# Kernel optimization log

Hardware: AMD Instinct MI355X
Metric: run time of the kernel (lower is better)

## Reference

```python
import jax, jax.numpy as jnp
import numpy as np
from jax.ops import segment_sum

N = 100000   # nodes
E = 1600000  # edges
D = 128      # input feature dim
H = 128      # hidden dim
S = 64       # substructure ids
G = 512      # graphs in batch
EPS = 1e-5


def setup_inputs() -> dict:
    key = jax.random.key(0)
    ks = jax.random.split(key, 12)
    subst_ids = jax.random.randint(ks[0], (N,), 0, S)
    x = jax.random.normal(ks[1], (N, D), dtype=jnp.float32)
    # column 5 carries the integer substructure id, as in data.x[:, 5].long()
    x = x.at[:, 5].set(subst_ids.astype(jnp.float32))
    edge_index = jax.random.randint(ks[2], (2, E), 0, N)
    batch = jnp.sort(jax.random.randint(ks[3], (N,), 0, G))
    s = 0.05  # weight scale to keep activations sane
    return {
        "x": x,
        "edge_index": edge_index,
        "subst_ids": subst_ids,
        "batch": batch,
        "attn_w1": jax.random.normal(ks[4], (D, 64), jnp.float32) * s,
        "attn_b1": jnp.zeros((64,), jnp.float32),
        "attn_w2": jax.random.normal(ks[5], (64, 1), jnp.float32) * s,
        "conv_w0": jax.random.normal(ks[6], (D + 1, H), jnp.float32) * s,
        "conv_b0": jnp.zeros((H,), jnp.float32),
        "conv_w1": jax.random.normal(ks[7], (H, H), jnp.float32) * s,
        "conv_b1": jnp.zeros((H,), jnp.float32),
        "conv_w2": jax.random.normal(ks[8], (H, H), jnp.float32) * s,
        "conv_b2": jnp.zeros((H,), jnp.float32),
        "conv_w3": jax.random.normal(ks[9], (H, H), jnp.float32) * s,
        "conv_b3": jnp.zeros((H,), jnp.float32),
        "bn_gamma": jnp.ones((4, H), jnp.float32),
        "bn_beta": jnp.zeros((4, H), jnp.float32),
        "bn_rmean": jnp.zeros((4, H), jnp.float32),
        "bn_rvar": jnp.ones((4, H), jnp.float32),
        "head_w1": jax.random.normal(ks[10], (H, H // 2), jnp.float32) * s,
        "head_b1": jnp.zeros((H // 2,), jnp.float32),
        "head_w2": jax.random.normal(ks[11], (H // 2, 1), jnp.float32) * s,
        "head_b2": jnp.zeros((1,), jnp.float32),
    }


def _gcn_conv(x, src, dst, dinv, w, b):
    # PyG GCNConv with self-loops: out[dst] += d^-1/2_src d^-1/2_dst (xW)[src]
    h = x @ w                                   # [N, H]
    coef = dinv[src] * dinv[dst]                # [E]
    agg = segment_sum(h[src] * coef[:, None], dst, num_segments=N)
    agg = agg + h * (dinv * dinv)[:, None]      # self-loop term
    return agg + b


def reference(x, edge_index, subst_ids, batch,
              attn_w1, attn_b1, attn_w2,
              conv_w0, conv_b0, conv_w1, conv_b1, conv_w2, conv_b2, conv_w3, conv_b3,
              bn_gamma, bn_beta, bn_rmean, bn_rvar,
              head_w1, head_b1, head_w2, head_b2):
    # --- substructure attention ---
    ones_n = jnp.ones((N,), x.dtype)
    cnt = jnp.maximum(segment_sum(ones_n, subst_ids, num_segments=S), 1.0)
    subst_mean = segment_sum(x, subst_ids, num_segments=S) / cnt[:, None]  # [S, D]
    scores = jnp.tanh(subst_mean @ attn_w1 + attn_b1) @ attn_w2            # [S, 1]
    subst_attn = jax.nn.softmax(scores, axis=0)                            # [S, 1]
    atom_attn = subst_attn[subst_ids]                                      # [N, 1]
    h = jnp.concatenate([x, atom_attn], axis=1)                            # [N, D+1]

    # --- shared symmetric normalization (self-loops included) ---
    src, dst = edge_index[0], edge_index[1]
    deg = segment_sum(jnp.ones((E,), x.dtype), dst, num_segments=N) + 1.0
    dinv = jax.lax.rsqrt(deg)

    convs = [(conv_w0, conv_b0), (conv_w1, conv_b1), (conv_w2, conv_b2), (conv_w3, conv_b3)]
    for i, (w, b) in enumerate(convs):
        h = _gcn_conv(h, src, dst, dinv, w, b)
        # BatchNorm1d in eval mode
        h = (h - bn_rmean[i]) * jax.lax.rsqrt(bn_rvar[i] + EPS) * bn_gamma[i] + bn_beta[i]
        h = jax.nn.elu(h) if i < 3 else jax.nn.relu(h)
        # dropout p=0.3 is identity in inference

    # --- global mean pool over graphs ---
    gcnt = jnp.maximum(segment_sum(jnp.ones((N,), x.dtype), batch, num_segments=G), 1.0)
    pooled = segment_sum(h, batch, num_segments=G) / gcnt[:, None]         # [G, H]

    # --- prediction head (dropout off) ---
    z = jax.nn.elu(pooled @ head_w1 + head_b1)
    return z @ head_w2 + head_b2                                            # [G, 1]
```

## Files before the change

### kernel.cpp

```cpp
#include <hip/hip_runtime.h>
#include <cmath>

#define NN 100000
#define EE 1600000
#define DD 128
#define HH 128
#define SS 64
#define GG 512

#define NBE 782
#define EBK 196
#define EHS 800

typedef float f32x4 __attribute__((ext_vector_type(4)));
typedef short s16x8 __attribute__((ext_vector_type(8)));

constexpr size_t alignup(size_t x){ return (x + 255) & ~(size_t)255; }
constexpr size_t SZ_P16   = (size_t)NN*64*sizeof(unsigned);
constexpr size_t OFF_HW   = 0;
constexpr size_t OFF_H    = alignup(OFF_HW + SZ_P16);
constexpr size_t OFF_CSRS = alignup(OFF_H + SZ_P16);
constexpr size_t OFF_ROW  = alignup(OFF_CSRS + (size_t)EE*4);
constexpr size_t OFF_DINV = alignup(OFF_ROW + (size_t)(NN+1)*4);
constexpr size_t OFF_SATT = alignup(OFF_DINV + (size_t)NN*4);
constexpr size_t OFF_GST  = alignup(OFF_SATT + 64*4);
constexpr size_t OFF_BH   = alignup(OFF_GST + 513*4);
constexpr size_t OFF_BO   = alignup(OFF_BH + (size_t)64*400*4);
constexpr size_t OFF_TOT  = alignup(OFF_BO + (size_t)64*400*4);
constexpr size_t OFF_ROW2 = alignup(OFF_TOT + 64*4);
constexpr size_t OFF_LIST = alignup(OFF_ROW2 + 65*4);
constexpr size_t OFF_W16  = alignup(OFF_LIST + (size_t)NN*4);
constexpr size_t OFF_EH   = alignup(OFF_W16 + (size_t)3*8192*4);
constexpr size_t OFF_EB   = alignup(OFF_EH + (size_t)EBK*EHS*4);
constexpr size_t OFF_ET   = alignup(OFF_EB + (size_t)EBK*EHS*4);
constexpr size_t OFF_EBASE= alignup(OFF_ET + EBK*4);
constexpr size_t OFF_DSTE = alignup(OFF_EBASE + 200*4);
constexpr size_t OFF_SRCE = alignup(OFF_DSTE + (size_t)EE*4);
constexpr size_t OFF_POOL = alignup(OFF_SRCE + (size_t)EE*4);
constexpr size_t OFF_GSUM = alignup(OFF_POOL + (size_t)GG*HH*4);
constexpr size_t OFF_END  = alignup(OFF_GSUM + (size_t)SS*DD*4);
constexpr size_t ZERO_BEG   = OFF_POOL;
constexpr size_t ZERO_BYTES = OFF_END - OFF_POOL;

__device__ __forceinline__ unsigned pack2bf(float a, float b){
  unsigned ua = __float_as_uint(a); ua += 0x7fffu + ((ua >> 16) & 1u);
  unsigned ub = __float_as_uint(b); ub += 0x7fffu + ((ub >> 16) & 1u);
  return (ua >> 16) | (ub & 0xffff0000u);
}
__device__ __forceinline__ float bf_lo(unsigned u){ return __uint_as_float(u << 16); }
__device__ __forceinline__ float bf_hi(unsigned u){ return __uint_as_float(u & 0xffff0000u); }
__device__ __forceinline__ s16x8 as_s16x8(uint4 v){ union { uint4 u; s16x8 s; } x; x.u = v; return x.s; }

__global__ __launch_bounds__(256) void hist_kernel(const int* __restrict__ sid, int* __restrict__ bhist)
{
  __shared__ int h[64];
  int t = threadIdx.x, b = blockIdx.x;
  if (t < 64) h[t] = 0;
  __syncthreads();
  int n = b*256 + t;
  if (n < NN) atomicAdd(&h[sid[n]], 1);
  __syncthreads();
  if (t < 64) bhist[t*400 + b] = h[t];
}

__global__ __launch_bounds__(512) void offs_kernel(const int* __restrict__ bhist, int* __restrict__ boff2, int* __restrict__ tots)
{
  __shared__ int sh[512];
  int s = blockIdx.x, t = threadIdx.x;
  int v = (t < 391) ? bhist[s*400 + t] : 0;
  sh[t] = v;
  __syncthreads();
  for (int off = 1; off < 512; off <<= 1) {
    int u = (t >= off) ? sh[t - off] : 0;
    __syncthreads();
    sh[t] += u;
    __syncthreads();
  }
  if (t < 391) boff2[s*400 + t] = sh[t] - v;
  if (t == 511) tots[s] = sh[511];
}

__global__ __launch_bounds__(64) void base_kernel(const int* __restrict__ tots, int* __restrict__ row2)
{
  int l = threadIdx.x;
  int v = tots[l];
  int xv = v;
  #pragma unroll
  for (int off = 1; off < 64; off <<= 1) {
    int u = __shfl_up(xv, off, 64);
    if (l >= off) xv += u;
  }
  row2[l] = xv - v;
  if (l == 63) row2[64] = xv;
}

__global__ __launch_bounds__(256) void fill2_kernel(
    const int* __restrict__ sid, const int* __restrict__ row2,
    const int* __restrict__ boff2, unsigned* __restrict__ list)
{
  __shared__ int h[64];
  int t = threadIdx.x, b = blockIdx.x;
  if (t < 64) h[t] = 0;
  __syncthreads();
  int n = b*256 + t;
  if (n < NN) {
    int s = sid[n];
    int lr = atomicAdd(&h[s], 1);
    int pos = row2[s] + boff2[s*400 + b] + lr;
    list[pos] = ((unsigned)s << 24) | (unsigned)n;
  }
}

__global__ __launch_bounds__(256) void subst_sum(
    const unsigned* __restrict__ list, const float* __restrict__ x,
    float* __restrict__ gsum)
{
  int b = blockIdx.x, t = threadIdx.x;
  int lane = t & 63, w = t >> 6;
  const int per = (NN + 1023)/1024;
  const int q   = (per + 3)/4;
  int bend = min(b*per + per, NN);
  int beg = b*per + w*q;
  int end = min(bend, beg + q);
  if (beg >= end) return;
  int d0 = lane * 2;
  float ax = 0.f, ay = 0.f;
  int scur = (int)(list[beg] >> 24);
  int i = beg;
  for (; i + 4 <= end; i += 4) {
    unsigned u0 = list[i], u1 = list[i+1], u2 = list[i+2], u3 = list[i+3];
    float2 v0 = *(const float2*)(x + (size_t)(u0 & 0xffffffu)*DD + d0);
    float2 v1 = *(const float2*)(x + (size_t)(u1 & 0xffffffu)*DD + d0);
    float2 v2 = *(const float2*)(x + (size_t)(u2 & 0xffffffu)*DD + d0);
    float2 v3 = *(const float2*)(x + (size_t)(u3 & 0xffffffu)*DD + d0);
    int s0 = u0 >> 24, s1 = u1 >> 24, s2 = u2 >> 24, s3 = u3 >> 24;
    if (s0 != scur) { atomicAdd(&gsum[scur*DD + d0], ax); atomicAdd(&gsum[scur*DD + d0 + 1], ay); scur = s0; ax = 0.f; ay = 0.f; }
    ax += v0.x; ay += v0.y;
    if (s1 != scur) { atomicAdd(&gsum[scur*DD + d0], ax); atomicAdd(&gsum[scur*DD + d0 + 1], ay); scur = s1; ax = 0.f; ay = 0.f; }
    ax += v1.x; ay += v1.y;
    if (s2 != scur) { atomicAdd(&gsum[scur*DD + d0], ax); atomicAdd(&gsum[scur*DD + d0 + 1], ay); scur = s2; ax = 0.f; ay = 0.f; }
    ax += v2.x; ay += v2.y;
    if (s3 != scur) { atomicAdd(&gsum[scur*DD + d0], ax); atomicAdd(&gsum[scur*DD + d0 + 1], ay); scur = s3; ax = 0.f; ay = 0.f; }
    ax += v3.x; ay += v3.y;
  }
  for (; i < end; ++i) {
    unsigned u = list[i];
    float2 v = *(const float2*)(x + (size_t)(u & 0xffffffu)*DD + d0);
    int s = u >> 24;
    if (s != scur) { atomicAdd(&gsum[scur*DD + d0], ax); atomicAdd(&gsum[scur*DD + d0 + 1], ay); scur = s; ax = 0.f; ay = 0.f; }
    ax += v.x; ay += v.y;
  }
  atomicAdd(&gsum[scur*DD + d0],     ax);
  atomicAdd(&gsum[scur*DD + d0 + 1], ay);
}

__global__ __launch_bounds__(1024) void attn_kernel(
    const float* __restrict__ g_sum, const int* __restrict__ row2,
    const float* __restrict__ w1, const float* __restrict__ b1,
    const float* __restrict__ w2, float* __restrict__ subst_attn)
{
  __shared__ float smean[SS*130];
  __shared__ float sw1[8192];
  __shared__ float sc[SS];
  int t = threadIdx.x;
  for (int i = t; i < SS*DD; i += 1024) {
    int s = i >> 7, d = i & 127;
    float c = fmaxf((float)(row2[s+1] - row2[s]), 1.0f);
    smean[s*130 + d] = g_sum[i] / c;
  }
  for (int i = t; i < 8192; i += 1024) sw1[i] = w1[i];
  __syncthreads();

  int s = t >> 4, jq = t & 15;
  float a0 = 0, a1 = 0, a2 = 0, a3 = 0;
  #pragma unroll 4
  for (int d = 0; d < 128; ++d) {
    float m = smean[s*130 + d];
    a0 += m * sw1[d*64 + jq     ];
    a1 += m * sw1[d*64 + jq + 16];
    a2 += m * sw1[d*64 + jq + 32];
    a3 += m * sw1[d*64 + jq + 48];
  }
  float acc = tanhf(a0 + b1[jq     ]) * w2[jq     ]
            + tanhf(a1 + b1[jq + 16]) * w2[jq + 16]
            + tanhf(a2 + b1[jq + 32]) * w2[jq + 32]
            + tanhf(a3 + b1[jq + 48]) * w2[jq + 48];
  acc += __shfl_xor(acc, 1, 64);
  acc += __shfl_xor(acc, 2, 64);
  acc += __shfl_xor(acc, 4, 64);
  acc += __shfl_xor(acc, 8, 64);
  if (jq == 0) sc[s] = acc;
  __syncthreads();
  if (t < 64) {
    float score = sc[t];
    float m = -1e30f;
    for (int i = 0; i < SS; ++i) m = fmaxf(m, sc[i]);
    float e = expf(score - m);
    float sum = 0.0f;
    for (int i = 0; i < SS; ++i) sum += expf(sc[i] - m);
    subst_attn[t] = e / sum;
  }
}

__global__ __launch_bounds__(256) void ehist_kernel(const int* __restrict__ dst, int* __restrict__ ehist)
{
  __shared__ int h[EBK];
  int t = threadIdx.x, b = blockIdx.x;
  if (t < EBK) h[t] = 0;
  __syncthreads();
  #pragma unroll
  for (int ii = 0; ii < 8; ++ii) {
    int e = b*2048 + ii*256 + t;
    if (e < EE) atomicAdd(&h[dst[e] >> 9], 1);
  }
  __syncthreads();
  if (t < EBK) ehist[t*EHS + b] = h[t];
}

__global__ __launch_bounds__(1024) void eoffs_kernel(const int* __restrict__ ehist, int* __restrict__ eboff, int* __restrict__ etots)
{
  __shared__ int sh[1024];
  int s = blockIdx.x, t = threadIdx.x;
  int v = (t < NBE) ? ehist[s*EHS + t] : 0;
  sh[t] = v;
  __syncthreads();
  for (int off = 1; off < 1024; off <<= 1) {
    int u = (t >= off) ? sh[t - off] : 0;
    __syncthreads();
    sh[t] += u;
    __syncthreads();
  }
  if (t < NBE) eboff[s*EHS + t] = sh[t] - v;
  if (t == 1023) etots[s] = sh[1023];
}

__global__ __launch_bounds__(256) void ebase_kernel(const int* __restrict__ etots, int* __restrict__ ebase)
{
  __shared__ int sh[256];
  int t = threadIdx.x;
  int v = (t < EBK) ? etots[t] : 0;
  sh[t] = v;
  __syncthreads();
  for (int off = 1; off < 256; off <<= 1) {
    int u = (t >= off) ? sh[t - off] : 0;
    __syncthreads();
    sh[t] += u;
    __syncthreads();
  }
  if (t < EBK) ebase[t] = sh[t] - v;
  if (t == EBK-1) ebase[EBK] = sh[t];
}

__global__ __launch_bounds__(256) void escat_kernel(
    const int* __restrict__ src, const int* __restrict__ dst,
    const int* __restrict__ ebase, const int* __restrict__ eboff,
    int* __restrict__ dste, int* __restrict__ srce)
{
  __shared__ int h[EBK];
  int t = threadIdx.x, b = blockIdx.x;
  if (t < EBK) h[t] = 0;
  __syncthreads();
  #pragma unroll
  for (int ii = 0; ii < 8; ++ii) {
    int e = b*2048 + ii*256 + t;
    if (e < EE) {
      int d = dst[e];
      int k = d >> 9;
      int lr = atomicAdd(&h[k], 1);
      int pos = ebase[k] + eboff[k*EHS + b] + lr;
      dste[pos] = d;
      srce[pos] = src[e];
    }
  }
}

__global__ __launch_bounds__(1024) void csr_build(
    const int* __restrict__ ebase, const int* __restrict__ dste, const int* __restrict__ srce,
    int* __restrict__ row_off, float* __restrict__ dinv, int* __restrict__ csr_src)
{
  __shared__ int scnt[512];
  __shared__ int sh[512];
  __shared__ int cur[512];
  int b = blockIdx.x, t = threadIdx.x;
  int base = ebase[b], cnt_b = ebase[b+1] - base;
  if (t < 512) scnt[t] = 0;
  __syncthreads();
  for (int i = t; i < cnt_b; i += 1024)
    atomicAdd(&scnt[dste[base + i] & 511], 1);
  __syncthreads();
  int orig = (t < 512) ? scnt[t] : 0;
  if (t < 512) sh[t] = orig;
  __syncthreads();
  for (int off = 1; off < 512; off <<= 1) {
    int u = (t < 512 && t >= off) ? sh[t - off] : 0;
    __syncthreads();
    if (t < 512) sh[t] += u;
    __syncthreads();
  }
  if (t < 512) {
    int excl = sh[t] - orig;
    int n = b*512 + t;
    if (n < NN) {
      row_off[n] = base + excl;
      dinv[n] = rsqrtf((float)(orig + 1));
    }
    cur[t] = excl;
  }
  if (b == EBK-1 && t == 0) row_off[NN] = EE;
  __syncthreads();
  for (int i = t; i < cnt_b; i += 1024) {
    int dl = dste[base + i] & 511;
    int pos = atomicAdd(&cur[dl], 1);
    csr_src[base + pos] = srce[base + i];
  }
}

__global__ __launch_bounds__(256) void gemm_kernel(
    const float* __restrict__ A, const float* __restrict__ W,
    unsigned* __restrict__ out,
    const int* __restrict__ sid, const float* __restrict__ sattn, int layer0)
{
  __shared__ float sA[32][129];
  __shared__ float sW[32][128];
  __shared__ float sExtra[128];
  __shared__ float sAttn[128];
  int tid = threadIdx.x;
  int tx = tid & 15, ty = tid >> 4;
  int row0 = blockIdx.x * 128;

  if (layer0) {
    if (tid < 128) sExtra[tid] = W[128*128 + tid];
    if (tid < 128) {
      int n = row0 + tid;
      sAttn[tid] = (n < NN) ? sattn[sid[n]] : 0.0f;
    }
  }

  float acc[8][8];
  #pragma unroll
  for (int i = 0; i < 8; ++i)
    #pragma unroll
    for (int j = 0; j < 8; ++j) acc[i][j] = 0.0f;

  for (int k0 = 0; k0 < 128; k0 += 32) {
    __syncthreads();
    #pragma unroll
    for (int p = 0; p < 4; ++p) {
      int q  = tid + 256*p;
      int r  = q >> 3;
      int kk = (q & 7) << 2;
      int n = row0 + r;
      float4 v = make_float4(0.f, 0.f, 0.f, 0.f);
      if (n < NN) v = *(const float4*)(A + (size_t)n*128 + k0 + kk);
      sA[kk+0][r] = v.x; sA[kk+1][r] = v.y; sA[kk+2][r] = v.z; sA[kk+3][r] = v.w;
    }
    #pragma unroll
    for (int p = 0; p < 4; ++p) {
      int q  = tid + 256*p;
      int kr = q >> 5;
      int c  = (q & 31) << 2;
      float4 v = *(const float4*)(W + (size_t)(k0 + kr)*128 + c);
      *(float4*)&sW[kr][c] = v;
    }
    __syncthreads();
    #pragma unroll 4
    for (int kk = 0; kk < 32; ++kk) {
      float av[8], wv[8];
      #pragma unroll
      for (int i = 0; i < 8; ++i) av[i] = sA[kk][ty*8 + i];
      #pragma unroll
      for (int j = 0; j < 8; ++j) wv[j] = sW[kk][tx*8 + j];
      #pragma unroll
      for (int i = 0; i < 8; ++i)
        #pragma unroll
        for (int j = 0; j < 8; ++j)
          acc[i][j] += av[i] * wv[j];
    }
  }

  if (layer0) {
    #pragma unroll
    for (int i = 0; i < 8; ++i) {
      float a = sAttn[ty*8 + i];
      #pragma unroll
      for (int j = 0; j < 8; ++j) acc[i][j] += a * sExtra[tx*8 + j];
    }
  }

  #pragma unroll
  for (int i = 0; i < 8; ++i) {
    int n = row0 + ty*8 + i;
    if (n < NN) {
      uint4 pk;
      pk.x = pack2bf(acc[i][0], acc[i][1]);
      pk.y = pack2bf(acc[i][2], acc[i][3]);
      pk.z = pack2bf(acc[i][4], acc[i][5]);
      pk.w = pack2bf(acc[i][6], acc[i][7]);
      *(uint4*)(out + (size_t)n*64 + tx*4) = pk;
    }
  }
}

__global__ __launch_bounds__(256) void packw_kernel(const float* __restrict__ W, unsigned* __restrict__ W16)
{
  int q = blockIdx.x*256 + threadIdx.x;
  int c = q & 127, kp = q >> 7;
  float f0 = W[(size_t)(2*kp  )*128 + c];
  float f1 = W[(size_t)(2*kp+1)*128 + c];
  W16[c*64 + kp] = pack2bf(f0, f1);
}

__global__ __launch_bounds__(256) void gemm16_kernel(
    const unsigned* __restrict__ A16, const unsigned* __restrict__ W16,
    unsigned* __restrict__ out)
{
  __shared__ unsigned lds[16384];
  int tid = threadIdx.x;
  int lane = tid & 63;
  int row0 = blockIdx.x * 128;

  #pragma unroll
  for (int p = 0; p < 8; ++p) {
    int q  = tid + 256*p;
    int r  = q >> 4;
    int ch = q & 15;
    int n = row0 + r;
    uint4 v = make_uint4(0u,0u,0u,0u);
    if (n < NN) v = *(const uint4*)(A16 + (size_t)n*64 + ch*4);
    int idx = (r*64 + ch*4) ^ ((r & 7) << 2);
    *(uint4*)&lds[idx] = v;
  }
  {
    const uint4* w4 = (const uint4*)W16;
    #pragma unroll
    for (int p = 0; p < 8; ++p) {
      int ch = tid + 256*p;
      int base = ch*4;
      int c = base >> 6;
      int idx = 8192 + (base ^ ((c & 7) << 2));
      *(uint4*)&lds[idx] = w4[ch];
    }
  }
  __syncthreads();

  int w = tid >> 6;
  int wrow = w * 32;
  int swz = (lane & 7) << 2;
  int kgrp = (lane >> 4) * 4;

  f32x4 acc0[8], acc1[8];
  #pragma unroll
  for (int j = 0; j < 8; ++j) { acc0[j] = (f32x4){0,0,0,0}; acc1[j] = (f32x4){0,0,0,0}; }

  #pragma unroll
  for (int kk = 0; kk < 4; ++kk) {
    int kbase = kk*16 + kgrp;
    int rowA0 = wrow + (lane & 15);
    int rowA1 = wrow + 16 + (lane & 15);
    uint4 avu0 = *(const uint4*)&lds[(rowA0*64 + kbase) ^ swz];
    uint4 avu1 = *(const uint4*)&lds[(rowA1*64 + kbase) ^ swz];
    s16x8 a0 = as_s16x8(avu0);
    s16x8 a1 = as_s16x8(avu1);
    #pragma unroll
    for (int j = 0; j < 8; ++j) {
      int col = j*16 + (lane & 15);
      uint4 bvu = *(const uint4*)&lds[8192 + ((col*64 + kbase) ^ swz)];
      s16x8 bfr = as_s16x8(bvu);
      acc0[j] = __builtin_amdgcn_mfma_f32_16x16x32_bf16(a0, bfr, acc0[j], 0, 0, 0);
      acc1[j] = __builtin_amdgcn_mfma_f32_16x16x32_bf16(a1, bfr, acc1[j], 0, 0, 0);
    }
  }
  __syncthreads();

  #pragma unroll
  for (int i2 = 0; i2 < 2; ++i2) {
    #pragma unroll
    for (int j = 0; j < 8; ++j) {
      f32x4 v = i2 ? acc1[j] : acc0[j];
      #pragma unroll
      for (int reg = 0; reg < 4; ++reg) {
        float own = v[reg];
        float part = __shfl_xor(own, 1, 64);
        if ((lane & 1) == 0) {
          int r  = wrow + i2*16 + (lane >> 4)*4 + reg;
          int cp = j*8 + ((lane & 15) >> 1);
          lds[r*68 + cp] = pack2bf(own, part);
        }
      }
    }
  }
  __syncthreads();

  #pragma unroll
  for (int p = 0; p < 8; ++p) {
    int q  = tid + 256*p;
    int r  = q >> 4;
    int ch = q & 15;
    int n = row0 + r;
    if (n < NN) {
      uint4 v = *(const uint4*)&lds[r*68 + ch*4];
      *(uint4*)(out + (size_t)n*64 + ch*4) = v;
    }
  }
}

__global__ __launch_bounds__(256) void gather_kernel(
    const unsigned* __restrict__ hw, const int* __restrict__ row_off,
    const int* __restrict__ csr_src,
    const float* __restrict__ dinv, const float* __restrict__ bias,
    const float* __restrict__ gma, const float* __restrict__ bta,
    const float* __restrict__ rmn, const float* __restrict__ rvr,
    unsigned* __restrict__ out, int relu_act)
{
  int w = (blockIdx.x*256 + threadIdx.x) >> 6;
  int lane = threadIdx.x & 63;
  int n0 = w * 2;
  if (n0 >= NN) return;
  n0 = __builtin_amdgcn_readfirstlane(n0);
  int n1 = n0 + 1;
  int j0 = lane * 2;

  float di0 = dinv[n0], di1 = dinv[n1];
  unsigned su0 = hw[(size_t)n0*64 + lane];
  unsigned su1 = hw[(size_t)n1*64 + lane];
  float ax0 = bf_lo(su0)*di0*di0, ay0 = bf_hi(su0)*di0*di0;
  float ax1 = bf_lo(su1)*di1*di1, ay1 = bf_hi(su1)*di1*di1;

  int b0 = __builtin_amdgcn_readfirstlane(row_off[n0]);
  int e0 = __builtin_amdgcn_readfirstlane(row_off[n0+1]);
  int e1 = __builtin_amdgcn_readfirstlane(row_off[n1+1]);
  int i0 = b0, i1 = e0;

  for (; i0 + 4 <= e0 && i1 + 4 <= e1; i0 += 4, i1 += 4) {
    int s00 = csr_src[i0+0], s01 = csr_src[i0+1], s02 = csr_src[i0+2], s03 = csr_src[i0+3];
    int s10 = csr_src[i1+0], s11 = csr_src[i1+1], s12 = csr_src[i1+2], s13 = csr_src[i1+3];
    unsigned u00 = hw[(size_t)s00*64 + lane];
    unsigned u01 = hw[(size_t)s01*64 + lane];
    unsigned u02 = hw[(size_t)s02*64 + lane];
    unsigned u03 = hw[(size_t)s03*64 + lane];
    unsigned u10 = hw[(size_t)s10*64 + lane];
    unsigned u11 = hw[(size_t)s11*64 + lane];
    unsigned u12 = hw[(size_t)s12*64 + lane];
    unsigned u13 = hw[(size_t)s13*64 + lane];
    float c00 = dinv[s00]*di0, c01 = dinv[s01]*di0, c02 = dinv[s02]*di0, c03 = dinv[s03]*di0;
    float c10 = dinv[s10]*di1, c11 = dinv[s11]*di1, c12 = dinv[s12]*di1, c13 = dinv[s13]*di1;
    ax0 += bf_lo(u00)*c00 + bf_lo(u01)*c01 + bf_lo(u02)*c02 + bf_lo(u03)*c03;
    ay0 += bf_hi(u00)*c00 + bf_hi(u01)*c01 + bf_hi(u02)*c02 + bf_hi(u03)*c03;
    ax1 += bf_lo(u10)*c10 + bf_lo(u11)*c11 + bf_lo(u12)*c12 + bf_lo(u13)*c13;
    ay1 += bf_hi(u10)*c10 + bf_hi(u11)*c11 + bf_hi(u12)*c12 + bf_hi(u13)*c13;
  }
  for (; i0 + 4 <= e0; i0 += 4) {
    int s0 = csr_src[i0+0], s1 = csr_src[i0+1], s2 = csr_src[i0+2], s3 = csr_src[i0+3];
    unsigned u0 = hw[(size_t)s0*64 + lane];
    unsigned u1 = hw[(size_t)s1*64 + lane];
    unsigned u2 = hw[(size_t)s2*64 + lane];
    unsigned u3 = hw[(size_t)s3*64 + lane];
    float c0 = dinv[s0]*di0, c1 = dinv[s1]*di0, c2 = dinv[s2]*di0, c3 = dinv[s3]*di0;
    ax0 += bf_lo(u0)*c0 + bf_lo(u1)*c1 + bf_lo(u2)*c2 + bf_lo(u3)*c3;
    ay0 += bf_hi(u0)*c0 + bf_hi(u1)*c1 + bf_hi(u2)*c2 + bf_hi(u3)*c3;
  }
  for (; i1 + 4 <= e1; i1 += 4) {
    int s0 = csr_src[i1+0], s1 = csr_src[i1+1], s2 = csr_src[i1+2], s3 = csr_src[i1+3];
    unsigned u0 = hw[(size_t)s0*64 + lane];
    unsigned u1 = hw[(size_t)s1*64 + lane];
    unsigned u2 = hw[(size_t)s2*64 + lane];
    unsigned u3 = hw[(size_t)s3*64 + lane];
    float c0 = dinv[s0]*di1, c1 = dinv[s1]*di1, c2 = dinv[s2]*di1, c3 = dinv[s3]*di1;
    ax1 += bf_lo(u0)*c0 + bf_lo(u1)*c1 + bf_lo(u2)*c2 + bf_lo(u3)*c3;
    ay1 += bf_hi(u0)*c0 + bf_hi(u1)*c1 + bf_hi(u2)*c2 + bf_hi(u3)*c3;
  }
  for (; i0 < e0; ++i0) {
    int s = csr_src[i0];
    float c = dinv[s]*di0;
    unsigned u = hw[(size_t)s*64 + lane];
    ax0 += bf_lo(u)*c; ay0 += bf_hi(u)*c;
  }
  for (; i1 < e1; ++i1) {
    int s = csr_src[i1];
    float c = dinv[s]*di1;
    unsigned u = hw[(size_t)s*64 + lane];
    ax1 += bf_lo(u)*c; ay1 += bf_hi(u)*c;
  }

  float iv0 = rsqrtf(rvr[j0]   + 1e-5f);
  float iv1 = rsqrtf(rvr[j0+1] + 1e-5f);
  float g0 = gma[j0], g1 = gma[j0+1];
  float m0 = rmn[j0], m1 = rmn[j0+1];
  float t0 = bta[j0], t1 = bta[j0+1];
  float bb0 = bias[j0], bb1 = bias[j0+1];

  float y00 = (ax0 + bb0 - m0) * iv0 * g0 + t0;
  float y01 = (ay0 + bb1 - m1) * iv1 * g1 + t1;
  float y10 = (ax1 + bb0 - m0) * iv0 * g0 + t0;
  float y11 = (ay1 + bb1 - m1) * iv1 * g1 + t1;
  if (relu_act) {
    y00 = fmaxf(y00, 0.0f); y01 = fmaxf(y01, 0.0f);
    y10 = fmaxf(y10, 0.0f); y11 = fmaxf(y11, 0.0f);
  } else {
    y00 = (y00 > 0.0f) ? y00 : expm1f(y00);
    y01 = (y01 > 0.0f) ? y01 : expm1f(y01);
    y10 = (y10 > 0.0f) ? y10 : expm1f(y10);
    y11 = (y11 > 0.0f) ? y11 : expm1f(y11);
  }
  out[(size_t)n0*64 + lane] = pack2bf(y00, y01);
  out[(size_t)n1*64 + lane] = pack2bf(y10, y11);
}

__global__ __launch_bounds__(256) void gstart_kernel(const int* __restrict__ batch, int* __restrict__ start)
{
  int n = blockIdx.x*256 + threadIdx.x;
  if (n >= NN) return;
  int b  = batch[n];
  int bp = (n == 0) ? -1 : batch[n-1];
  for (int g = bp + 1; g <= b; ++g) start[g] = n;
  if (n == NN-1) {
    for (int g = b + 1; g <= GG; ++g) start[g] = NN;
  }
}

__global__ __launch_bounds__(256) void pool_kernel(
    const unsigned* __restrict__ h16, const int* __restrict__ batch, float* __restrict__ pooled)
{
  int wave = (blockIdx.x*256 + threadIdx.x) >> 6;
  int lane = threadIdx.x & 63;
  const int CH = 64;
  int beg = wave * CH;
  if (beg >= NN) return;
  int end = min(beg + CH, NN);
  int j0 = lane * 2;
  float ax = 0.f, ay = 0.f;
  int gcur = batch[beg];
  for (int n = beg; n < end; ++n) {
    int g = batch[n];
    if (g != gcur) {
      atomicAdd(&pooled[(size_t)gcur*128 + j0],     ax);
      atomicAdd(&pooled[(size_t)gcur*128 + j0 + 1], ay);
      ax = 0.f; ay = 0.f; gcur = g;
    }
    unsigned u = h16[(size_t)n*64 + lane];
    ax += bf_lo(u); ay += bf_hi(u);
  }
  atomicAdd(&pooled[(size_t)gcur*128 + j0],     ax);
  atomicAdd(&pooled[(size_t)gcur*128 + j0 + 1], ay);
}

__global__ __launch_bounds__(64) void head_kernel(
    const float* __restrict__ pooled, const int* __restrict__ start,
    const float* __restrict__ w1, const float* __restrict__ b1,
    const float* __restrict__ w2, const float* __restrict__ b2,
    float* __restrict__ out)
{
  __shared__ float p[128];
  int g = blockIdx.x;
  int t = threadIdx.x;
  float cnt = fmaxf((float)(start[g+1] - start[g]), 1.0f);
  p[t]      = pooled[(size_t)g*128 + t]      / cnt;
  p[t + 64] = pooled[(size_t)g*128 + t + 64] / cnt;
  __syncthreads();
  float a = 0.f;
  #pragma unroll 4
  for (int d = 0; d < 128; ++d) a += p[d] * w1[d*64 + t];
  float z = a + b1[t];
  z = (z > 0.f) ? z : expm1f(z);
  float v = z * w2[t];
  #pragma unroll
  for (int off = 32; off > 0; off >>= 1) v += __shfl_down(v, off, 64);
  if (t == 0) out[g] = v + b2[0];
}

extern "C" void kernel_launch(void* const* d_in, const int* in_sizes, int n_in,
                              void* d_out, int out_size, void* d_ws, size_t ws_size,
                              hipStream_t stream)
{
  const float* x        = (const float*)d_in[0];
  const int*   eidx     = (const int*)d_in[1];
  const int*   sid      = (const int*)d_in[2];
  const int*   batch    = (const int*)d_in[3];
  const float* attn_w1  = (const float*)d_in[4];
  const float* attn_b1  = (const float*)d_in[5];
  const float* attn_w2  = (const float*)d_in[6];
  const float* conv_w[4] = {(const float*)d_in[7], (const float*)d_in[9],
                            (const float*)d_in[11], (const float*)d_in[13]};
  const float* conv_b[4] = {(const float*)d_in[8], (const float*)d_in[10],
                            (const float*)d_in[12], (const float*)d_in[14]};
  const float* bn_gamma = (const float*)d_in[15];
  const float* bn_beta  = (const float*)d_in[16];
  const float* bn_rmean = (const float*)d_in[17];
  const float* bn_rvar  = (const float*)d_in[18];
  const float* head_w1  = (const float*)d_in[19];
  const float* head_b1  = (const float*)d_in[20];
  const float* head_w2  = (const float*)d_in[21];
  const float* head_b2  = (const float*)d_in[22];
  float* out = (float*)d_out;

  char* ws = (char*)d_ws;
  unsigned* hw16  = (unsigned*)(ws + OFF_HW);
  unsigned* h16   = (unsigned*)(ws + OFF_H);
  int*   csr_src  = (int*)  (ws + OFF_CSRS);
  int*   row_off  = (int*)  (ws + OFF_ROW);
  float* dinv     = (float*)(ws + OFF_DINV);
  float* sattn    = (float*)(ws + OFF_SATT);
  int*   gstart   = (int*)  (ws + OFF_GST);
  int*   bhist    = (int*)  (ws + OFF_BH);
  int*   boff2    = (int*)  (ws + OFF_BO);
  int*   tots     = (int*)  (ws + OFF_TOT);
  int*   row2     = (int*)  (ws + OFF_ROW2);
  unsigned* list  = (unsigned*)(ws + OFF_LIST);
  unsigned* w16   = (unsigned*)(ws + OFF_W16);
  int*   ehist    = (int*)  (ws + OFF_EH);
  int*   eboff    = (int*)  (ws + OFF_EB);
  int*   etots    = (int*)  (ws + OFF_ET);
  int*   ebase    = (int*)  (ws + OFF_EBASE);
  int*   dste     = (int*)  (ws + OFF_DSTE);
  int*   srce     = (int*)  (ws + OFF_SRCE);
  float* pooled   = (float*)(ws + OFF_POOL);
  float* gsum     = (float*)(ws + OFF_GSUM);

  const int* e_src = eidx;
  const int* e_dst = eidx + EE;

  hipMemsetAsync(ws + ZERO_BEG, 0, ZERO_BYTES, stream);

  int nb256 = (NN + 255)/256;

  hist_kernel <<<nb256, 256, 0, stream>>>(sid, bhist);
  offs_kernel <<<64, 512, 0, stream>>>(bhist, boff2, tots);
  base_kernel <<<1, 64, 0, stream>>>(tots, row2);
  fill2_kernel<<<nb256, 256, 0, stream>>>(sid, row2, boff2, list);
  subst_sum   <<<1024, 256, 0, stream>>>(list, x, gsum);
  attn_kernel <<<1, 1024, 0, stream>>>(gsum, row2, attn_w1, attn_b1, attn_w2, sattn);

  ehist_kernel<<<NBE, 256, 0, stream>>>(e_dst, ehist);
  eoffs_kernel<<<EBK, 1024, 0, stream>>>(ehist, eboff, etots);
  ebase_kernel<<<1, 256, 0, stream>>>(etots, ebase);
  escat_kernel<<<NBE, 256, 0, stream>>>(e_src, e_dst, ebase, eboff, dste, srce);
  csr_build   <<<EBK, 1024, 0, stream>>>(ebase, dste, srce, row_off, dinv, csr_src);

  gstart_kernel<<<nb256, 256, 0, stream>>>(batch, gstart);

  for (int L = 1; L < 4; ++L)
    packw_kernel<<<32, 256, 0, stream>>>(conv_w[L], w16 + (size_t)(L-1)*8192);

  int gemm_grid = (NN + 127)/128;
  int gat_grid  = ((NN/2)*64 + 255)/256;
  for (int L = 0; L < 4; ++L) {
    if (L == 0)
      gemm_kernel<<<gemm_grid, 256, 0, stream>>>(x, conv_w[0], hw16, sid, sattn, 1);
    else
      gemm16_kernel<<<gemm_grid, 256, 0, stream>>>(h16, w16 + (size_t)(L-1)*8192, hw16);
    gather_kernel<<<gat_grid, 256, 0, stream>>>(hw16, row_off, csr_src, dinv,
        conv_b[L], bn_gamma + L*HH, bn_beta + L*HH, bn_rmean + L*HH, bn_rvar + L*HH,
        h16, (L == 3) ? 1 : 0);
  }

  int pool_waves  = (NN + 63)/64;
  int pool_blocks = (pool_waves + 3)/4;
  pool_kernel<<<pool_blocks, 256, 0, stream>>>(h16, batch, pooled);
  head_kernel<<<GG, 64, 0, stream>>>(pooled, gstart, head_w1, head_b1, head_w2, head_b2, out);
}
```

Before: 537.8 us.

## Store features in 8 column slices so gathers hit cache-resident slices

Hidden features move from a row-major bf16 layout to 8 column slices of 16 features each, every slice holding all nodes contiguously. The gather kernel is rebuilt so each block handles one slice for 32 nodes, with 8 nodes per wave and 8 lanes per node. This shrinks the random-access working set per slice (about 3.2 MB) so it can stay in cache during the edge gather. The GEMMs and pooling read and write the new layout. In exchange each gather access is only 32 bytes per node, and CSR indices and dinv are reread 8 times, once per slice.

```diff
diff --git a/kernel.cpp b/kernel.cpp
--- a/kernel.cpp
+++ b/kernel.cpp
@@ -317,7 +317,7 @@
 
 __global__ __launch_bounds__(256) void gemm_kernel(
     const float* __restrict__ A, const float* __restrict__ W,
-    unsigned* __restrict__ out,
+    unsigned* __restrict__ out8,
     const int* __restrict__ sid, const float* __restrict__ sattn, int layer0)
 {
   __shared__ float sA[32][129];
@@ -396,7 +396,7 @@
       pk.y = pack2bf(acc[i][2], acc[i][3]);
       pk.z = pack2bf(acc[i][4], acc[i][5]);
       pk.w = pack2bf(acc[i][6], acc[i][7]);
-      *(uint4*)(out + (size_t)n*64 + tx*4) = pk;
+      *(uint4*)(out8 + ((size_t)(tx >> 1)*NN + n)*8 + (tx & 1)*4) = pk;
     }
   }
 }
@@ -411,8 +411,8 @@
 }
 
 __global__ __launch_bounds__(256) void gemm16_kernel(
-    const unsigned* __restrict__ A16, const unsigned* __restrict__ W16,
-    unsigned* __restrict__ out)
+    const unsigned* __restrict__ A8, const unsigned* __restrict__ W16,
+    unsigned* __restrict__ out8)
 {
   __shared__ unsigned lds[16384];
   int tid = threadIdx.x;
@@ -426,7 +426,7 @@
     int ch = q & 15;
     int n = row0 + r;
     uint4 v = make_uint4(0u,0u,0u,0u);
-    if (n < NN) v = *(const uint4*)(A16 + (size_t)n*64 + ch*4);
+    if (n < NN) v = *(const uint4*)(A8 + ((size_t)(ch >> 1)*NN + n)*8 + (ch & 1)*4);
     int idx = (r*64 + ch*4) ^ ((r & 7) << 2);
     *(uint4*)&lds[idx] = v;
   }
@@ -499,111 +499,62 @@
     int n = row0 + r;
     if (n < NN) {
       uint4 v = *(const uint4*)&lds[r*68 + ch*4];
-      *(uint4*)(out + (size_t)n*64 + ch*4) = v;
-    }
-  }
-}
-
-__global__ __launch_bounds__(256) void gather_kernel(
-    const unsigned* __restrict__ hw, const int* __restrict__ row_off,
-    const int* __restrict__ csr_src,
-    const float* __restrict__ dinv, const float* __restrict__ bias,
+      *(uint4*)(out8 + ((size_t)(ch >> 1)*NN + n)*8 + (ch & 1)*4) = v;
+    }
+  }
+}
+
+__global__ __launch_bounds__(256) void gather8_kernel(
+    const unsigned* __restrict__ hw8, const int* __restrict__ row_off,
+    const int* __restrict__ csr_src, const float* __restrict__ dinv,
+    const float* __restrict__ bias,
     const float* __restrict__ gma, const float* __restrict__ bta,
     const float* __restrict__ rmn, const float* __restrict__ rvr,
-    unsigned* __restrict__ out, int relu_act)
-{
-  int w = (blockIdx.x*256 + threadIdx.x) >> 6;
+    unsigned* __restrict__ out8, int relu_act)
+{
+  int slice = blockIdx.x & 7;
+  int chunk = blockIdx.x >> 3;
+  int wv   = threadIdx.x >> 6;
   int lane = threadIdx.x & 63;
-  int n0 = w * 2;
-  if (n0 >= NN) return;
-  n0 = __builtin_amdgcn_readfirstlane(n0);
-  int n1 = n0 + 1;
-  int j0 = lane * 2;
-
-  float di0 = dinv[n0], di1 = dinv[n1];
-  unsigned su0 = hw[(size_t)n0*64 + lane];
-  unsigned su1 = hw[(size_t)n1*64 + lane];
-  float ax0 = bf_lo(su0)*di0*di0, ay0 = bf_hi(su0)*di0*di0;
-  float ax1 = bf_lo(su1)*di1*di1, ay1 = bf_hi(su1)*di1*di1;
-
-  int b0 = __builtin_amdgcn_readfirstlane(row_off[n0]);
-  int e0 = __builtin_amdgcn_readfirstlane(row_off[n0+1]);
-  int e1 = __builtin_amdgcn_readfirstlane(row_off[n1+1]);
-  int i0 = b0, i1 = e0;
-
-  for (; i0 + 4 <= e0 && i1 + 4 <= e1; i0 += 4, i1 += 4) {
-    int s00 = csr_src[i0+0], s01 = csr_src[i0+1], s02 = csr_src[i0+2], s03 = csr_src[i0+3];
-    int s10 = csr_src[i1+0], s11 = csr_src[i1+1], s12 = csr_src[i1+2], s13 = csr_src[i1+3];
-    unsigned u00 = hw[(size_t)s00*64 + lane];
-    unsigned u01 = hw[(size_t)s01*64 + lane];
-    unsigned u02 = hw[(size_t)s02*64 + lane];
-    unsigned u03 = hw[(size_t)s03*64 + lane];
-    unsigned u10 = hw[(size_t)s10*64 + lane];
-    unsigned u11 = hw[(size_t)s11*64 + lane];
-    unsigned u12 = hw[(size_t)s12*64 + lane];
-    unsigned u13 = hw[(size_t)s13*64 + lane];
-    float c00 = dinv[s00]*di0, c01 = dinv[s01]*di0, c02 = dinv[s02]*di0, c03 = dinv[s03]*di0;
-    float c10 = dinv[s10]*di1, c11 = dinv[s11]*di1, c12 = dinv[s12]*di1, c13 = dinv[s13]*di1;
-    ax0 += bf_lo(u00)*c00 + bf_lo(u01)*c01 + bf_lo(u02)*c02 + bf_lo(u03)*c03;
-    ay0 += bf_hi(u00)*c00 + bf_hi(u01)*c01 + bf_hi(u02)*c02 + bf_hi(u03)*c03;
-    ax1 += bf_lo(u10)*c10 + bf_lo(u11)*c11 + bf_lo(u12)*c12 + bf_lo(u13)*c13;
-    ay1 += bf_hi(u10)*c10 + bf_hi(u11)*c11 + bf_hi(u12)*c12 + bf_hi(u13)*c13;
-  }
-  for (; i0 + 4 <= e0; i0 += 4) {
-    int s0 = csr_src[i0+0], s1 = csr_src[i0+1], s2 = csr_src[i0+2], s3 = csr_src[i0+3];
-    unsigned u0 = hw[(size_t)s0*64 + lane];
-    unsigned u1 = hw[(size_t)s1*64 + lane];
-    unsigned u2 = hw[(size_t)s2*64 + lane];
-    unsigned u3 = hw[(size_t)s3*64 + lane];
-    float c0 = dinv[s0]*di0, c1 = dinv[s1]*di0, c2 = dinv[s2]*di0, c3 = dinv[s3]*di0;
-    ax0 += bf_lo(u0)*c0 + bf_lo(u1)*c1 + bf_lo(u2)*c2 + bf_lo(u3)*c3;
-    ay0 += bf_hi(u0)*c0 + bf_hi(u1)*c1 + bf_hi(u2)*c2 + bf_hi(u3)*c3;
-  }
-  for (; i1 + 4 <= e1; i1 += 4) {
-    int s0 = csr_src[i1+0], s1 = csr_src[i1+1], s2 = csr_src[i1+2], s3 = csr_src[i1+3];
-    unsigned u0 = hw[(size_t)s0*64 + lane];
-    unsigned u1 = hw[(size_t)s1*64 + lane];
-    unsigned u2 = hw[(size_t)s2*64 + lane];
-    unsigned u3 = hw[(size_t)s3*64 + lane];
-    float c0 = dinv[s0]*di1, c1 = dinv[s1]*di1, c2 = dinv[s2]*di1, c3 = dinv[s3]*di1;
-    ax1 += bf_lo(u0)*c0 + bf_lo(u1)*c1 + bf_lo(u2)*c2 + bf_lo(u3)*c3;
-    ay1 += bf_hi(u0)*c0 + bf_hi(u1)*c1 + bf_hi(u2)*c2 + bf_hi(u3)*c3;
-  }
-  for (; i0 < e0; ++i0) {
-    int s = csr_src[i0];
-    float c = dinv[s]*di0;
-    unsigned u = hw[(size_t)s*64 + lane];
-    ax0 += bf_lo(u)*c; ay0 += bf_hi(u)*c;
-  }
-  for (; i1 < e1; ++i1) {
-    int s = csr_src[i1];
-    float c = dinv[s]*di1;
-    unsigned u = hw[(size_t)s*64 + lane];
-    ax1 += bf_lo(u)*c; ay1 += bf_hi(u)*c;
-  }
-
+  int ns = lane >> 3;
+  int u  = lane & 7;
+  int n = chunk*32 + wv*8 + ns;
+  const unsigned* hws = hw8 + (size_t)slice*NN*8;
+
+  float di = dinv[n];
+  unsigned su = hws[(size_t)n*8 + u];
+  float ax = bf_lo(su)*di*di, ay = bf_hi(su)*di*di;
+
+  int beg = row_off[n], end = row_off[n+1];
+  int i = beg;
+  for (; i + 2 <= end; i += 2) {
+    int s0 = csr_src[i], s1 = csr_src[i+1];
+    unsigned u0 = hws[(size_t)s0*8 + u];
+    unsigned u1 = hws[(size_t)s1*8 + u];
+    float c0 = dinv[s0]*di, c1 = dinv[s1]*di;
+    ax += bf_lo(u0)*c0 + bf_lo(u1)*c1;
+    ay += bf_hi(u0)*c0 + bf_hi(u1)*c1;
+  }
+  if (i < end) {
+    int s = csr_src[i];
+    unsigned uu = hws[(size_t)s*8 + u];
+    float c = dinv[s]*di;
+    ax += bf_lo(uu)*c; ay += bf_hi(uu)*c;
+  }
+
+  int j0 = slice*16 + u*2;
   float iv0 = rsqrtf(rvr[j0]   + 1e-5f);
   float iv1 = rsqrtf(rvr[j0+1] + 1e-5f);
-  float g0 = gma[j0], g1 = gma[j0+1];
-  float m0 = rmn[j0], m1 = rmn[j0+1];
-  float t0 = bta[j0], t1 = bta[j0+1];
-  float bb0 = bias[j0], bb1 = bias[j0+1];
-
-  float y00 = (ax0 + bb0 - m0) * iv0 * g0 + t0;
-  float y01 = (ay0 + bb1 - m1) * iv1 * g1 + t1;
-  float y10 = (ax1 + bb0 - m0) * iv0 * g0 + t0;
-  float y11 = (ay1 + bb1 - m1) * iv1 * g1 + t1;
+  float y0 = (ax + bias[j0]   - rmn[j0]  ) * iv0 * gma[j0]   + bta[j0];
+  float y1 = (ay + bias[j0+1] - rmn[j0+1]) * iv1 * gma[j0+1] + bta[j0+1];
   if (relu_act) {
-    y00 = fmaxf(y00, 0.0f); y01 = fmaxf(y01, 0.0f);
-    y10 = fmaxf(y10, 0.0f); y11 = fmaxf(y11, 0.0f);
+    y0 = fmaxf(y0, 0.0f);
+    y1 = fmaxf(y1, 0.0f);
   } else {
-    y00 = (y00 > 0.0f) ? y00 : expm1f(y00);
-    y01 = (y01 > 0.0f) ? y01 : expm1f(y01);
-    y10 = (y10 > 0.0f) ? y10 : expm1f(y10);
-    y11 = (y11 > 0.0f) ? y11 : expm1f(y11);
-  }
-  out[(size_t)n0*64 + lane] = pack2bf(y00, y01);
-  out[(size_t)n1*64 + lane] = pack2bf(y10, y11);
+    y0 = (y0 > 0.0f) ? y0 : expm1f(y0);
+    y1 = (y1 > 0.0f) ? y1 : expm1f(y1);
+  }
+  out8[((size_t)slice*NN + n)*8 + u] = pack2bf(y0, y1);
 }
 
 __global__ __launch_bounds__(256) void gstart_kernel(const int* __restrict__ batch, int* __restrict__ start)
@@ -619,7 +570,7 @@
 }
 
 __global__ __launch_bounds__(256) void pool_kernel(
-    const unsigned* __restrict__ h16, const int* __restrict__ batch, float* __restrict__ pooled)
+    const unsigned* __restrict__ h8, const int* __restrict__ batch, float* __restrict__ pooled)
 {
   int wave = (blockIdx.x*256 + threadIdx.x) >> 6;
   int lane = threadIdx.x & 63;
@@ -627,7 +578,10 @@
   int beg = wave * CH;
   if (beg >= NN) return;
   int end = min(beg + CH, NN);
-  int j0 = lane * 2;
+  int slice = lane >> 3;
+  int u = lane & 7;
+  int j0 = slice*16 + u*2;
+  const unsigned* hs = h8 + (size_t)slice*NN*8;
   float ax = 0.f, ay = 0.f;
   int gcur = batch[beg];
   for (int n = beg; n < end; ++n) {
@@ -637,8 +591,8 @@
       atomicAdd(&pooled[(size_t)gcur*128 + j0 + 1], ay);
       ax = 0.f; ay = 0.f; gcur = g;
     }
-    unsigned u = h16[(size_t)n*64 + lane];
-    ax += bf_lo(u); ay += bf_hi(u);
+    unsigned uu = hs[(size_t)n*8 + u];
+    ax += bf_lo(uu); ay += bf_hi(uu);
   }
   atomicAdd(&pooled[(size_t)gcur*128 + j0],     ax);
   atomicAdd(&pooled[(size_t)gcur*128 + j0 + 1], ay);
@@ -694,8 +648,8 @@
   float* out = (float*)d_out;
 
   char* ws = (char*)d_ws;
-  unsigned* hw16  = (unsigned*)(ws + OFF_HW);
-  unsigned* h16   = (unsigned*)(ws + OFF_H);
+  unsigned* hw8   = (unsigned*)(ws + OFF_HW);
+  unsigned* h8    = (unsigned*)(ws + OFF_H);
   int*   csr_src  = (int*)  (ws + OFF_CSRS);
   int*   row_off  = (int*)  (ws + OFF_ROW);
   float* dinv     = (float*)(ws + OFF_DINV);
@@ -742,19 +696,19 @@
     packw_kernel<<<32, 256, 0, stream>>>(conv_w[L], w16 + (size_t)(L-1)*8192);
 
   int gemm_grid = (NN + 127)/128;
-  int gat_grid  = ((NN/2)*64 + 255)/256;
+  int gat_grid  = (NN/32) * 8;
   for (int L = 0; L < 4; ++L) {
     if (L == 0)
-      gemm_kernel<<<gemm_grid, 256, 0, stream>>>(x, conv_w[0], hw16, sid, sattn, 1);
+      gemm_kernel<<<gemm_grid, 256, 0, stream>>>(x, conv_w[0], hw8, sid, sattn, 1);
     else
-      gemm16_kernel<<<gemm_grid, 256, 0, stream>>>(h16, w16 + (size_t)(L-1)*8192, hw16);
-    gather_kernel<<<gat_grid, 256, 0, stream>>>(hw16, row_off, csr_src, dinv,
+      gemm16_kernel<<<gemm_grid, 256, 0, stream>>>(h8, w16 + (size_t)(L-1)*8192, hw8);
+    gather8_kernel<<<gat_grid, 256, 0, stream>>>(hw8, row_off, csr_src, dinv,
         conv_b[L], bn_gamma + L*HH, bn_beta + L*HH, bn_rmean + L*HH, bn_rvar + L*HH,
-        h16, (L == 3) ? 1 : 0);
+        h8, (L == 3) ? 1 : 0);
   }
 
   int pool_waves  = (NN + 63)/64;
   int pool_blocks = (pool_waves + 3)/4;
-  pool_kernel<<<pool_blocks, 256, 0, stream>>>(h16, batch, pooled);
+  pool_kernel<<<pool_blocks, 256, 0, stream>>>(h8, batch, pooled);
   head_kernel<<<GG, 64, 0, stream>>>(pooled, gstart, head_w1, head_b1, head_w2, head_b2, out);
 }
```

After: 881.4 us. +63.9%, slower.

## Run layer-0 GEMM on bf16 MFMA path and pack edge scatter into one word

Applied to the files above, without the earlier changes.

The fp32 scalar layer-0 GEMM is removed. The input x is converted to bf16 by a new pack kernel, and layer 0 now uses the MFMA-based gemm16 kernel, with the attention-column rank-1 term folded into its epilogue. Separately, the edge scatter stores the local destination and the source in one packed 32-bit word instead of two arrays, which halves scatter and CSR-build traffic. Rounding x to bf16 adds some precision loss, and the packed format assumes source ids fit in 17 bits.

```diff
diff --git a/kernel.cpp b/kernel.cpp
--- a/kernel.cpp
+++ b/kernel.cpp
@@ -19,7 +19,8 @@
 constexpr size_t SZ_P16   = (size_t)NN*64*sizeof(unsigned);
 constexpr size_t OFF_HW   = 0;
 constexpr size_t OFF_H    = alignup(OFF_HW + SZ_P16);
-constexpr size_t OFF_CSRS = alignup(OFF_H + SZ_P16);
+constexpr size_t OFF_X16  = alignup(OFF_H + SZ_P16);
+constexpr size_t OFF_CSRS = alignup(OFF_X16 + SZ_P16);
 constexpr size_t OFF_ROW  = alignup(OFF_CSRS + (size_t)EE*4);
 constexpr size_t OFF_DINV = alignup(OFF_ROW + (size_t)(NN+1)*4);
 constexpr size_t OFF_SATT = alignup(OFF_DINV + (size_t)NN*4);
@@ -30,13 +31,12 @@
 constexpr size_t OFF_ROW2 = alignup(OFF_TOT + 64*4);
 constexpr size_t OFF_LIST = alignup(OFF_ROW2 + 65*4);
 constexpr size_t OFF_W16  = alignup(OFF_LIST + (size_t)NN*4);
-constexpr size_t OFF_EH   = alignup(OFF_W16 + (size_t)3*8192*4);
+constexpr size_t OFF_EH   = alignup(OFF_W16 + (size_t)4*8192*4);
 constexpr size_t OFF_EB   = alignup(OFF_EH + (size_t)EBK*EHS*4);
 constexpr size_t OFF_ET   = alignup(OFF_EB + (size_t)EBK*EHS*4);
 constexpr size_t OFF_EBASE= alignup(OFF_ET + EBK*4);
-constexpr size_t OFF_DSTE = alignup(OFF_EBASE + 200*4);
-constexpr size_t OFF_SRCE = alignup(OFF_DSTE + (size_t)EE*4);
-constexpr size_t OFF_POOL = alignup(OFF_SRCE + (size_t)EE*4);
+constexpr size_t OFF_EPK  = alignup(OFF_EBASE + 200*4);
+constexpr size_t OFF_POOL = alignup(OFF_EPK + (size_t)EE*4);
 constexpr size_t OFF_GSUM = alignup(OFF_POOL + (size_t)GG*HH*4);
 constexpr size_t OFF_END  = alignup(OFF_GSUM + (size_t)SS*DD*4);
 constexpr size_t ZERO_BEG   = OFF_POOL;
@@ -254,7 +254,7 @@
 __global__ __launch_bounds__(256) void escat_kernel(
     const int* __restrict__ src, const int* __restrict__ dst,
     const int* __restrict__ ebase, const int* __restrict__ eboff,
-    int* __restrict__ dste, int* __restrict__ srce)
+    unsigned* __restrict__ epk)
 {
   __shared__ int h[EBK];
   int t = threadIdx.x, b = blockIdx.x;
@@ -268,14 +268,13 @@
       int k = d >> 9;
       int lr = atomicAdd(&h[k], 1);
       int pos = ebase[k] + eboff[k*EHS + b] + lr;
-      dste[pos] = d;
-      srce[pos] = src[e];
+      epk[pos] = ((unsigned)(d & 511) << 17) | (unsigned)src[e];
     }
   }
 }
 
 __global__ __launch_bounds__(1024) void csr_build(
-    const int* __restrict__ ebase, const int* __restrict__ dste, const int* __restrict__ srce,
+    const int* __restrict__ ebase, const unsigned* __restrict__ epk,
     int* __restrict__ row_off, float* __restrict__ dinv, int* __restrict__ csr_src)
 {
   __shared__ int scnt[512];
@@ -286,7 +285,7 @@
   if (t < 512) scnt[t] = 0;
   __syncthreads();
   for (int i = t; i < cnt_b; i += 1024)
-    atomicAdd(&scnt[dste[base + i] & 511], 1);
+    atomicAdd(&scnt[epk[base + i] >> 17], 1);
   __syncthreads();
   int orig = (t < 512) ? scnt[t] : 0;
   if (t < 512) sh[t] = orig;
@@ -309,96 +308,24 @@
   if (b == EBK-1 && t == 0) row_off[NN] = EE;
   __syncthreads();
   for (int i = t; i < cnt_b; i += 1024) {
-    int dl = dste[base + i] & 511;
+    unsigned en = epk[base + i];
+    int dl = en >> 17;
     int pos = atomicAdd(&cur[dl], 1);
-    csr_src[base + pos] = srce[base + i];
-  }
-}
-
-__global__ __launch_bounds__(256) void gemm_kernel(
-    const float* __restrict__ A, const float* __restrict__ W,
-    unsigned* __restrict__ out,
-    const int* __restrict__ sid, const float* __restrict__ sattn, int layer0)
-{
-  __shared__ float sA[32][129];
-  __shared__ float sW[32][128];
-  __shared__ float sExtra[128];
-  __shared__ float sAttn[128];
-  int tid = threadIdx.x;
-  int tx = tid & 15, ty = tid >> 4;
-  int row0 = blockIdx.x * 128;
-
-  if (layer0) {
-    if (tid < 128) sExtra[tid] = W[128*128 + tid];
-    if (tid < 128) {
-      int n = row0 + tid;
-      sAttn[tid] = (n < NN) ? sattn[sid[n]] : 0.0f;
-    }
-  }
-
-  float acc[8][8];
-  #pragma unroll
-  for (int i = 0; i < 8; ++i)
-    #pragma unroll
-    for (int j = 0; j < 8; ++j) acc[i][j] = 0.0f;
-
-  for (int k0 = 0; k0 < 128; k0 += 32) {
-    __syncthreads();
-    #pragma unroll
-    for (int p = 0; p < 4; ++p) {
-      int q  = tid + 256*p;
-      int r  = q >> 3;
-      int kk = (q & 7) << 2;
-      int n = row0 + r;
-      float4 v = make_float4(0.f, 0.f, 0.f, 0.f);
-      if (n < NN) v = *(const float4*)(A + (size_t)n*128 + k0 + kk);
-      sA[kk+0][r] = v.x; sA[kk+1][r] = v.y; sA[kk+2][r] = v.z; sA[kk+3][r] = v.w;
-    }
-    #pragma unroll
-    for (int p = 0; p < 4; ++p) {
-      int q  = tid + 256*p;
-      int kr = q >> 5;
-      int c  = (q & 31) << 2;
-      float4 v = *(const float4*)(W + (size_t)(k0 + kr)*128 + c);
-      *(float4*)&sW[kr][c] = v;
-    }
-    __syncthreads();
-    #pragma unroll 4
-    for (int kk = 0; kk < 32; ++kk) {
-      float av[8], wv[8];
-      #pragma unroll
-      for (int i = 0; i < 8; ++i) av[i] = sA[kk][ty*8 + i];
-      #pragma unroll
-      for (int j = 0; j < 8; ++j) wv[j] = sW[kk][tx*8 + j];
-      #pragma unroll
-      for (int i = 0; i < 8; ++i)
-        #pragma unroll
-        for (int j = 0; j < 8; ++j)
-          acc[i][j] += av[i] * wv[j];
-    }
-  }
-
-  if (layer0) {
-    #pragma unroll
-    for (int i = 0; i < 8; ++i) {
-      float a = sAttn[ty*8 + i];
-      #pragma unroll
-      for (int j = 0; j < 8; ++j) acc[i][j] += a * sExtra[tx*8 + j];
-    }
-  }
-
-  #pragma unroll
-  for (int i = 0; i < 8; ++i) {
-    int n = row0 + ty*8 + i;
-    if (n < NN) {
-      uint4 pk;
-      pk.x = pack2bf(acc[i][0], acc[i][1]);
-      pk.y = pack2bf(acc[i][2], acc[i][3]);
-      pk.z = pack2bf(acc[i][4], acc[i][5]);
-      pk.w = pack2bf(acc[i][6], acc[i][7]);
-      *(uint4*)(out + (size_t)n*64 + tx*4) = pk;
-    }
-  }
+    csr_src[base + pos] = (int)(en & 0x1FFFFu);
+  }
+}
+
+__global__ __launch_bounds__(256) void packx_kernel(const float* __restrict__ x, unsigned* __restrict__ x16)
+{
+  int q = blockIdx.x*256 + threadIdx.x;
+  const float4* xf = (const float4*)x;
+  float4 f0 = xf[q*2], f1 = xf[q*2+1];
+  uint4 pk;
+  pk.x = pack2bf(f0.x, f0.y);
+  pk.y = pack2bf(f0.z, f0.w);
+  pk.z = pack2bf(f1.x, f1.y);
+  pk.w = pack2bf(f1.z, f1.w);
+  *(uint4*)(x16 + (size_t)q*4) = pk;
 }
 
 __global__ __launch_bounds__(256) void packw_kernel(const float* __restrict__ W, unsigned* __restrict__ W16)
@@ -412,12 +339,22 @@
 
 __global__ __launch_bounds__(256) void gemm16_kernel(
     const unsigned* __restrict__ A16, const unsigned* __restrict__ W16,
-    unsigned* __restrict__ out)
+    unsigned* __restrict__ out,
+    const int* __restrict__ sid, const float* __restrict__ sattn,
+    const float* __restrict__ wextra, int layer0)
 {
   __shared__ unsigned lds[16384];
+  __shared__ float sAttn[128];
+  __shared__ float sExtra[128];
   int tid = threadIdx.x;
   int lane = tid & 63;
   int row0 = blockIdx.x * 128;
+
+  if (layer0 && tid < 128) {
+    int n = row0 + tid;
+    sAttn[tid]  = (n < NN) ? sattn[sid[n]] : 0.0f;
+    sExtra[tid] = wextra[tid];
+  }
 
   #pragma unroll
   for (int p = 0; p < 8; ++p) {
@@ -480,9 +417,13 @@
       #pragma unroll
       for (int reg = 0; reg < 4; ++reg) {
         float own = v[reg];
+        int r  = wrow + i2*16 + (lane >> 4)*4 + reg;
+        if (layer0) {
+          int col = j*16 + (lane & 15);
+          own += sAttn[r] * sExtra[col];
+        }
         float part = __shfl_xor(own, 1, 64);
         if ((lane & 1) == 0) {
-          int r  = wrow + i2*16 + (lane >> 4)*4 + reg;
           int cp = j*8 + ((lane & 15) >> 1);
           lds[r*68 + cp] = pack2bf(own, part);
         }
@@ -696,6 +637,7 @@
   char* ws = (char*)d_ws;
   unsigned* hw16  = (unsigned*)(ws + OFF_HW);
   unsigned* h16   = (unsigned*)(ws + OFF_H);
+  unsigned* x16   = (unsigned*)(ws + OFF_X16);
   int*   csr_src  = (int*)  (ws + OFF_CSRS);
   int*   row_off  = (int*)  (ws + OFF_ROW);
   float* dinv     = (float*)(ws + OFF_DINV);
@@ -711,8 +653,7 @@
   int*   eboff    = (int*)  (ws + OFF_EB);
   int*   etots    = (int*)  (ws + OFF_ET);
   int*   ebase    = (int*)  (ws + OFF_EBASE);
-  int*   dste     = (int*)  (ws + OFF_DSTE);
-  int*   srce     = (int*)  (ws + OFF_SRCE);
+  unsigned* epk   = (unsigned*)(ws + OFF_EPK);
   float* pooled   = (float*)(ws + OFF_POOL);
   float* gsum     = (float*)(ws + OFF_GSUM);
 
@@ -733,21 +674,21 @@
   ehist_kernel<<<NBE, 256, 0, stream>>>(e_dst, ehist);
   eoffs_kernel<<<EBK, 1024, 0, stream>>>(ehist, eboff, etots);
   ebase_kernel<<<1, 256, 0, stream>>>(etots, ebase);
-  escat_kernel<<<NBE, 256, 0, stream>>>(e_src, e_dst, ebase, eboff, dste, srce);
-  csr_build   <<<EBK, 1024, 0, stream>>>(ebase, dste, srce, row_off, dinv, csr_src);
+  escat_kernel<<<NBE, 256, 0, stream>>>(e_src, e_dst, ebase, eboff, epk);
+  csr_build   <<<EBK, 1024, 0, stream>>>(ebase, epk, row_off, dinv, csr_src);
 
   gstart_kernel<<<nb256, 256, 0, stream>>>(batch, gstart);
 
-  for (int L = 1; L < 4; ++L)
-    packw_kernel<<<32, 256, 0, stream>>>(conv_w[L], w16 + (size_t)(L-1)*8192);
+  packx_kernel<<<(NN*16)/256, 256, 0, stream>>>(x, x16);
+  for (int L = 0; L < 4; ++L)
+    packw_kernel<<<32, 256, 0, stream>>>(conv_w[L], w16 + (size_t)L*8192);
 
   int gemm_grid = (NN + 127)/128;
   int gat_grid  = ((NN/2)*64 + 255)/256;
   for (int L = 0; L < 4; ++L) {
-    if (L == 0)
-      gemm_kernel<<<gemm_grid, 256, 0, stream>>>(x, conv_w[0], hw16, sid, sattn, 1);
-    else
-      gemm16_kernel<<<gemm_grid, 256, 0, stream>>>(h16, w16 + (size_t)(L-1)*8192, hw16);
+    const unsigned* A = (L == 0) ? x16 : h16;
+    gemm16_kernel<<<gemm_grid, 256, 0, stream>>>(A, w16 + (size_t)L*8192, hw16,
+        sid, sattn, conv_w[0] + 128*128, (L == 0) ? 1 : 0);
     gather_kernel<<<gat_grid, 256, 0, stream>>>(hw16, row_off, csr_src, dinv,
         conv_b[L], bn_gamma + L*HH, bn_beta + L*HH, bn_rmean + L*HH, bn_rvar + L*HH,
         h16, (L == 3) ? 1 : 0);
```

Measured after the change: 514.3 us. 1.05x faster.
